# Performance work log

Measured on AMD Instinct MI355X. Metric: run time of the kernel, lower is better.

Reference implementation:

```python
import jax, jax.numpy as jnp
import numpy as np

N, E, DIN, DOUT = 50000, 500000, 128, 128


def setup_inputs() -> dict:
    key = jax.random.key(0)
    ks = jax.random.split(key, 12)
    s = 0.02
    return {
        "x": jax.random.normal(ks[0], (N, DIN), jnp.float32),
        "pos": jax.random.normal(ks[1], (N, 3), jnp.float32),
        "edge_index": jax.random.randint(ks[2], (2, E), 0, N, jnp.int64),
        # mlp_h: Linear(DIN,DIN) -> ReLU -> Linear(DIN,3) -> Tanh
        "h_w1": jax.random.normal(ks[3], (DIN, DIN), jnp.float32) * s,
        "h_b1": jnp.zeros((DIN,), jnp.float32),
        "h_w2": jax.random.normal(ks[4], (DIN, 3), jnp.float32) * s,
        "h_b2": jnp.zeros((3,), jnp.float32),
        # mlp_f: Linear(DIN+3, DOUT) -> ReLU
        "f_w": jax.random.normal(ks[5], (DIN + 3, DOUT), jnp.float32) * s,
        "f_b": jnp.zeros((DOUT,), jnp.float32),
        # mlp_g: Linear(DOUT,DOUT) -> ReLU -> Linear(DOUT,DIN) -> ReLU
        "g_w1": jax.random.normal(ks[6], (DOUT, DOUT), jnp.float32) * s,
        "g_b1": jnp.zeros((DOUT,), jnp.float32),
        "g_w2": jax.random.normal(ks[7], (DOUT, DIN), jnp.float32) * s,
        "g_b2": jnp.zeros((DIN,), jnp.float32),
    }


def reference(x, pos, edge_index, h_w1, h_b1, h_w2, h_b2, f_w, f_b,
              g_w1, g_b1, g_w2, g_b2):
    # PointGNNConv (aggr='sum'):
    #   delta = mlp_h(x)                                   [N, 3]
    #   msg_e = mlp_f([pos_j - pos_i + delta_i, x_j])      [E, DOUT]
    #   agg_i = sum_{j in N(i)} msg_e                       [N, DOUT]
    #   out   = x + mlp_g(agg)                              [N, DIN]
    delta = jnp.tanh(jax.nn.relu(x @ h_w1 + h_b1) @ h_w2 + h_b2)
    src = edge_index[0]  # j (source)
    dst = edge_index[1]  # i (target)
    edge_feat = jnp.concatenate(
        [pos[src] - pos[dst] + delta[dst], x[src]], axis=-1)  # [E, DIN+3]
    msg = jax.nn.relu(edge_feat @ f_w + f_b)                   # [E, DOUT]
    agg = jax.ops.segment_sum(msg, dst, num_segments=N)        # [N, DOUT]
    out = jax.nn.relu(jax.nn.relu(agg @ g_w1 + g_b1) @ g_w2 + g_b2)
    return x + out
```

## Files before the change

kernel.cpp:

```cpp
#include <hip/hip_runtime.h>
#include <hip/hip_bf16.h>

typedef float f32x4 __attribute__((ext_vector_type(4)));
typedef short bf16x8 __attribute__((ext_vector_type(8)));
typedef unsigned short u16x8 __attribute__((ext_vector_type(8)));

#define MFMA16(a, b, c) __builtin_amdgcn_mfma_f32_16x16x32_bf16((a), (b), (c), 0, 0, 0)
#define BCAP 128

static __device__ __forceinline__ short f2bf(float f) {
    union { float f; unsigned u; } v; v.f = f;
    unsigned r = v.u + 0x7FFFu + ((v.u >> 16) & 1u);
    return (short)(r >> 16);
}
static __device__ __forceinline__ float bflo(unsigned u) {
    union { unsigned u; float f; } v; v.u = u << 16; return v.f;
}
static __device__ __forceinline__ float bfhi(unsigned u) {
    union { unsigned u; float f; } v; v.u = u & 0xffff0000u; return v.f;
}
static __device__ __forceinline__ unsigned packbf(float lo, float hi) {
    return ((unsigned)(unsigned short)f2bf(lo)) | (((unsigned)(unsigned short)f2bf(hi)) << 16);
}

__global__ __launch_bounds__(256) void k_prep(
    const float* __restrict__ hw1, const float* __restrict__ fw,
    const float* __restrict__ gw1, const float* __restrict__ gw2,
    unsigned short* __restrict__ wT,
    const int* __restrict__ ei, int* __restrict__ flag,
    int* __restrict__ cursor, int N)
{
    const int gtid = blockIdx.x * 256 + threadIdx.x;
    if (gtid == 0) {
        int nz = 0;
        for (int i = 0; i < 64; ++i) nz |= ei[2 * i + 1];
        *flag = (nz != 0) ? 1 : 0;
    }
    for (int i = gtid; i < N; i += 16384) cursor[i] = i << 7;
    const int idx = gtid;
    const int c = idx >> 7, k = idx & 127;
    wT[0 * 16384 + idx] = (unsigned short)f2bf(hw1[(size_t)k * 128 + c]);
    wT[1 * 16384 + idx] = (unsigned short)f2bf(fw[(size_t)(3 + k) * 128 + c]);
    wT[2 * 16384 + idx] = (unsigned short)f2bf(gw1[(size_t)k * 128 + c]);
    wT[3 * 16384 + idx] = (unsigned short)f2bf(gw2[(size_t)k * 128 + c]);
}

static __device__ __forceinline__ void scatter_edges(
    const int* __restrict__ ei, int* __restrict__ cursor, int* __restrict__ list,
    int f, int E, int gbase, int gstride)
{
    const int stride2 = gstride * 2;
    for (int e0 = gbase * 2; e0 < E; e0 += stride2) {
        int s0, s1 = 0, d0, d1 = 0;
        const bool two = (e0 + 1 < E);
        if (f) {
            if (two) {
                const int2 sv = *reinterpret_cast<const int2*>(ei + e0);
                const int2 dv = *reinterpret_cast<const int2*>(ei + (size_t)E + e0);
                s0 = sv.x; s1 = sv.y; d0 = dv.x; d1 = dv.y;
            } else { s0 = ei[e0]; d0 = ei[(size_t)E + e0]; }
        } else {
            if (two) {
                const int4 sv = *reinterpret_cast<const int4*>(ei + 2 * (size_t)e0);
                const int4 dv = *reinterpret_cast<const int4*>(ei + 2 * ((size_t)E + e0));
                s0 = sv.x; s1 = sv.z; d0 = dv.x; d1 = dv.z;
            } else { s0 = ei[2 * (size_t)e0]; d0 = ei[2 * ((size_t)E + e0)]; }
        }
        int p = atomicAdd(&cursor[d0], 1);
        if (p < (d0 << 7) + BCAP) list[p] = s0;
        if (two) {
            p = atomicAdd(&cursor[d1], 1);
            if (p < (d1 << 7) + BCAP) list[p] = s1;
        }
    }
}

__global__ __launch_bounds__(256) void k_front(
    const float* __restrict__ x, const float* __restrict__ pos,
    const float* __restrict__ hb1,
    const float* __restrict__ hw2, const float* __restrict__ hb2,
    const float* __restrict__ fw, const float* __restrict__ fb,
    const unsigned short* __restrict__ wT,
    unsigned short* __restrict__ Pb, unsigned short* __restrict__ Qb, int N,
    const int* __restrict__ ei, int* __restrict__ cursor, int* __restrict__ list,
    const int* __restrict__ flag, int E)
{
    __shared__ float t1s[16][132];
    __shared__ unsigned short pls[16 * 128];
    __shared__ float poss[48];
    __shared__ float dqs[48];
    __shared__ float w2s[384];
    __shared__ float w3s[384];
    __shared__ float b1s[128], fbs[128], b2s[3];

    const int tid = threadIdx.x;
    const int lane = tid & 63, wave = tid >> 6;
    const int r16 = lane & 15, kg = lane >> 4;
    const int f = *flag;
    const bool early = (blockIdx.x & 1);

    for (int i = tid; i < 128; i += 256) { b1s[i] = hb1[i]; fbs[i] = fb[i]; }
    for (int i = tid; i < 384; i += 256) { w2s[i] = hw2[i]; w3s[i] = fw[i]; }
    if (tid < 3) b2s[tid] = hb2[tid];

    const unsigned short* hw1T = wT;
    const unsigned short* fwxT = wT + 16384;
    bf16x8 bw1[2][4], bwx[2][4];
    #pragma unroll
    for (int si = 0; si < 2; ++si) {
        const int c = (wave * 2 + si) * 16 + r16;
        #pragma unroll
        for (int t = 0; t < 4; ++t) {
            const int k0 = t * 32 + kg * 8;
            bw1[si][t] = *reinterpret_cast<const bf16x8*>(hw1T + c * 128 + k0);
            bwx[si][t] = *reinterpret_cast<const bf16x8*>(fwxT + c * 128 + k0);
        }
    }

    const int ntiles = (N + 15) >> 4;
    int tile = blockIdx.x;

    float4 px[8];
    float posr = 0.f;
    if (tile < ntiles) {
        int arow = (tile << 4) + r16; if (arow >= N) arow = N - 1;
        const float4* p = reinterpret_cast<const float4*>(x + (size_t)arow * 128);
        #pragma unroll
        for (int t = 0; t < 4; ++t) { px[2 * t] = p[t * 8 + kg * 2]; px[2 * t + 1] = p[t * 8 + kg * 2 + 1]; }
        if (tid < 48) {
            int r = tid / 3, m = tid - 3 * r;
            int rr = (tile << 4) + r; if (rr >= N) rr = N - 1;
            posr = pos[(size_t)rr * 3 + m];
        }
    }

    if (early)
        scatter_edges(ei, cursor, list, f, E, blockIdx.x * 256 + tid, gridDim.x * 256);

    __syncthreads();

    for (; tile < ntiles; tile += gridDim.x) {
        const int row0 = tile << 4;

        if (tid < 48) poss[tid] = posr;
        bf16x8 a[4];
        #pragma unroll
        for (int t = 0; t < 4; ++t) {
            float4 u0 = px[2 * t], u1 = px[2 * t + 1];
            bf16x8 v;
            v[0] = f2bf(u0.x); v[1] = f2bf(u0.y); v[2] = f2bf(u0.z); v[3] = f2bf(u0.w);
            v[4] = f2bf(u1.x); v[5] = f2bf(u1.y); v[6] = f2bf(u1.z); v[7] = f2bf(u1.w);
            a[t] = v;
        }
        const int ntile = tile + gridDim.x;
        if (ntile < ntiles) {
            int arow = (ntile << 4) + r16; if (arow >= N) arow = N - 1;
            const float4* p = reinterpret_cast<const float4*>(x + (size_t)arow * 128);
            #pragma unroll
            for (int t = 0; t < 4; ++t) { px[2 * t] = p[t * 8 + kg * 2]; px[2 * t + 1] = p[t * 8 + kg * 2 + 1]; }
            if (tid < 48) {
                int r = tid / 3, m = tid - 3 * r;
                int rr = (ntile << 4) + r; if (rr >= N) rr = N - 1;
                posr = pos[(size_t)rr * 3 + m];
            }
        }
        f32x4 acc1[2], accP[2];
        acc1[0] = 0.f; acc1[1] = 0.f; accP[0] = 0.f; accP[1] = 0.f;
        #pragma unroll
        for (int t = 0; t < 4; ++t) {
            #pragma unroll
            for (int si = 0; si < 2; ++si) {
                acc1[si] = MFMA16(a[t], bw1[si][t], acc1[si]);
                accP[si] = MFMA16(a[t], bwx[si][t], accP[si]);
            }
        }
        #pragma unroll
        for (int si = 0; si < 2; ++si) {
            const int c = (wave * 2 + si) * 16 + r16;
            #pragma unroll
            for (int j = 0; j < 4; ++j) {
                const int r = kg * 4 + j;
                t1s[r][c] = fmaxf(acc1[si][j] + b1s[c], 0.f);
            }
        }
        __syncthreads();

        #pragma unroll
        for (int si = 0; si < 2; ++si) {
            const int c = (wave * 2 + si) * 16 + r16;
            const int g = c >> 3, ce = c & 7;
            #pragma unroll
            for (int j = 0; j < 4; ++j) {
                const int r = kg * 4 + j;
                float pval = accP[si][j] + fbs[c]
                    + poss[r * 3 + 0] * w3s[0 * 128 + c]
                    + poss[r * 3 + 1] * w3s[1 * 128 + c]
                    + poss[r * 3 + 2] * w3s[2 * 128 + c];
                pls[r * 128 + (g ^ r) * 8 + ce] = (unsigned short)f2bf(pval);
            }
        }
        if (tid < 192) {
            const int pair = tid >> 2, h = tid & 3;
            const int r = pair / 3, m = pair - 3 * r;
            float s = 0.f;
            const int k0 = h * 32;
            #pragma unroll
            for (int k = k0; k < k0 + 32; k += 4) {
                float4 tv = *reinterpret_cast<const float4*>(&t1s[r][k]);
                s += tv.x * w2s[(k + 0) * 3 + m] + tv.y * w2s[(k + 1) * 3 + m]
                   + tv.z * w2s[(k + 2) * 3 + m] + tv.w * w2s[(k + 3) * 3 + m];
            }
            s += __shfl_xor(s, 1, 4);
            s += __shfl_xor(s, 2, 4);
            if (h == 0) dqs[pair] = tanhf(s + b2s[m]) - poss[pair];
        }
        __syncthreads();

        {
            const int row = tid >> 4, g0 = tid & 15;
            if (row0 + row < N) {
                u16x8 v = *reinterpret_cast<const u16x8*>(&pls[row * 128 + (g0 ^ row) * 8]);
                *reinterpret_cast<u16x8*>(Pb + (size_t)(row0 + row) * 128 + g0 * 8) = v;
            }
        }
        #pragma unroll
        for (int it = 0; it < 2; ++it) {
            const int idx = tid + it * 256;
            const int cg = idx & 31, r = idx >> 5;
            const int c0 = cg * 4;
            if (row0 + r < N) {
                const float d0 = dqs[r * 3 + 0], d1 = dqs[r * 3 + 1], d2 = dqs[r * 3 + 2];
                float q0 = d0 * w3s[c0 + 0] + d1 * w3s[128 + c0 + 0] + d2 * w3s[256 + c0 + 0];
                float q1 = d0 * w3s[c0 + 1] + d1 * w3s[128 + c0 + 1] + d2 * w3s[256 + c0 + 1];
                float q2 = d0 * w3s[c0 + 2] + d1 * w3s[128 + c0 + 2] + d2 * w3s[256 + c0 + 2];
                float q3 = d0 * w3s[c0 + 3] + d1 * w3s[128 + c0 + 3] + d2 * w3s[256 + c0 + 3];
                uint2 w; w.x = packbf(q0, q1); w.y = packbf(q2, q3);
                *reinterpret_cast<uint2*>(Qb + (size_t)(row0 + r) * 128 + c0) = w;
            }
        }
        __syncthreads();
    }

    if (!early)
        scatter_edges(ei, cursor, list, f, E, blockIdx.x * 256 + tid, gridDim.x * 256);
}

__global__ __launch_bounds__(256) void k_agg(
    const unsigned short* __restrict__ Pb, const unsigned short* __restrict__ Qb,
    const int* __restrict__ cursor, const int* __restrict__ list,
    unsigned short* __restrict__ aggb, int N)
{
    const int d = blockIdx.x * 16 + (threadIdx.x >> 4);
    if (d >= N) return;
    const int l = threadIdx.x & 15;
    const int start = d << 7;
    const int deg = min(cursor[d] - start, BCAP);

    const uint4 qu = *reinterpret_cast<const uint4*>(Qb + (size_t)d * 128 + l * 8);
    const float q0 = bflo(qu.x), q1 = bfhi(qu.x), q2 = bflo(qu.y), q3 = bfhi(qu.y);
    const float q4 = bflo(qu.z), q5 = bfhi(qu.z), q6 = bflo(qu.w), q7 = bfhi(qu.w);
    float a0 = 0.f, a1 = 0.f, a2 = 0.f, a3 = 0.f;
    float a4 = 0.f, a5 = 0.f, a6 = 0.f, a7 = 0.f;

#define ACC_EDGE(u) do { \
        a0 += fmaxf(bflo(u.x) + q0, 0.f); \
        a1 += fmaxf(bfhi(u.x) + q1, 0.f); \
        a2 += fmaxf(bflo(u.y) + q2, 0.f); \
        a3 += fmaxf(bfhi(u.y) + q3, 0.f); \
        a4 += fmaxf(bflo(u.z) + q4, 0.f); \
        a5 += fmaxf(bfhi(u.z) + q5, 0.f); \
        a6 += fmaxf(bflo(u.w) + q6, 0.f); \
        a7 += fmaxf(bfhi(u.w) + q7, 0.f); \
    } while (0)

    for (int b0 = 0; b0 < deg; b0 += 16) {
        int s = 0;
        if (b0 + l < deg) s = list[start + b0 + l];
        const int m = min(16, deg - b0);
        int k = 0;
        for (; k + 8 <= m; k += 8) {
            const int sj0 = __shfl(s, k + 0, 16);
            const int sj1 = __shfl(s, k + 1, 16);
            const int sj2 = __shfl(s, k + 2, 16);
            const int sj3 = __shfl(s, k + 3, 16);
            const int sj4 = __shfl(s, k + 4, 16);
            const int sj5 = __shfl(s, k + 5, 16);
            const int sj6 = __shfl(s, k + 6, 16);
            const int sj7 = __shfl(s, k + 7, 16);
            const uint4 u0 = *reinterpret_cast<const uint4*>(Pb + (size_t)sj0 * 128 + l * 8);
            const uint4 u1 = *reinterpret_cast<const uint4*>(Pb + (size_t)sj1 * 128 + l * 8);
            const uint4 u2 = *reinterpret_cast<const uint4*>(Pb + (size_t)sj2 * 128 + l * 8);
            const uint4 u3 = *reinterpret_cast<const uint4*>(Pb + (size_t)sj3 * 128 + l * 8);
            const uint4 u4 = *reinterpret_cast<const uint4*>(Pb + (size_t)sj4 * 128 + l * 8);
            const uint4 u5 = *reinterpret_cast<const uint4*>(Pb + (size_t)sj5 * 128 + l * 8);
            const uint4 u6 = *reinterpret_cast<const uint4*>(Pb + (size_t)sj6 * 128 + l * 8);
            const uint4 u7 = *reinterpret_cast<const uint4*>(Pb + (size_t)sj7 * 128 + l * 8);
            ACC_EDGE(u0); ACC_EDGE(u1); ACC_EDGE(u2); ACC_EDGE(u3);
            ACC_EDGE(u4); ACC_EDGE(u5); ACC_EDGE(u6); ACC_EDGE(u7);
        }
        for (; k + 4 <= m; k += 4) {
            const int sj0 = __shfl(s, k + 0, 16);
            const int sj1 = __shfl(s, k + 1, 16);
            const int sj2 = __shfl(s, k + 2, 16);
            const int sj3 = __shfl(s, k + 3, 16);
            const uint4 u0 = *reinterpret_cast<const uint4*>(Pb + (size_t)sj0 * 128 + l * 8);
            const uint4 u1 = *reinterpret_cast<const uint4*>(Pb + (size_t)sj1 * 128 + l * 8);
            const uint4 u2 = *reinterpret_cast<const uint4*>(Pb + (size_t)sj2 * 128 + l * 8);
            const uint4 u3 = *reinterpret_cast<const uint4*>(Pb + (size_t)sj3 * 128 + l * 8);
            ACC_EDGE(u0); ACC_EDGE(u1); ACC_EDGE(u2); ACC_EDGE(u3);
        }
        for (; k < m; ++k) {
            const int sj = __shfl(s, k, 16);
            const uint4 u = *reinterpret_cast<const uint4*>(Pb + (size_t)sj * 128 + l * 8);
            ACC_EDGE(u);
        }
    }
#undef ACC_EDGE

    uint4 w;
    w.x = packbf(a0, a1); w.y = packbf(a2, a3);
    w.z = packbf(a4, a5); w.w = packbf(a6, a7);
    *reinterpret_cast<uint4*>(aggb + (size_t)d * 128 + l * 8) = w;
}

__global__ __launch_bounds__(256) void k_back(
    const unsigned short* __restrict__ aggb, const float* __restrict__ x,
    const unsigned short* __restrict__ wT,
    const float* __restrict__ gb1, const float* __restrict__ gb2,
    float* __restrict__ out, int N)
{
    __shared__ unsigned short uls[16 * 128];
    __shared__ float b1s[128], b2s[128];

    const int tid = threadIdx.x;
    const int lane = tid & 63, wave = tid >> 6;
    const int r16 = lane & 15, kg = lane >> 4;

    for (int i = tid; i < 128; i += 256) { b1s[i] = gb1[i]; b2s[i] = gb2[i]; }

    const unsigned short* gw1T = wT + 2 * 16384;
    const unsigned short* gw2T = wT + 3 * 16384;
    bf16x8 bg1[2][4], bg2[2][4];
    #pragma unroll
    for (int si = 0; si < 2; ++si) {
        const int c = (wave * 2 + si) * 16 + r16;
        #pragma unroll
        for (int t = 0; t < 4; ++t) {
            const int k0 = t * 32 + kg * 8;
            bg1[si][t] = *reinterpret_cast<const bf16x8*>(gw1T + c * 128 + k0);
            bg2[si][t] = *reinterpret_cast<const bf16x8*>(gw2T + c * 128 + k0);
        }
    }

    const int ntiles = (N + 15) >> 4;
    int tile = blockIdx.x;

    bf16x8 a[4];
    float xv[2][4];
    if (tile < ntiles) {
        int arow = (tile << 4) + r16; if (arow >= N) arow = N - 1;
        #pragma unroll
        for (int t = 0; t < 4; ++t)
            a[t] = *reinterpret_cast<const bf16x8*>(aggb + (size_t)arow * 128 + t * 32 + kg * 8);
        #pragma unroll
        for (int si = 0; si < 2; ++si) {
            const int c = (wave * 2 + si) * 16 + r16;
            #pragma unroll
            for (int j = 0; j < 4; ++j) {
                const int r = (tile << 4) + kg * 4 + j;
                xv[si][j] = (r < N) ? x[(size_t)r * 128 + c] : 0.f;
            }
        }
    }
    __syncthreads();

    for (; tile < ntiles; tile += gridDim.x) {
        const int row0 = tile << 4;

        f32x4 accU[2];
        accU[0] = 0.f; accU[1] = 0.f;
        #pragma unroll
        for (int t = 0; t < 4; ++t) {
            #pragma unroll
            for (int si = 0; si < 2; ++si)
                accU[si] = MFMA16(a[t], bg1[si][t], accU[si]);
        }

        const int ntile = tile + gridDim.x;
        float xvn[2][4];
        if (ntile < ntiles) {
            int arow = (ntile << 4) + r16; if (arow >= N) arow = N - 1;
            #pragma unroll
            for (int t = 0; t < 4; ++t)
                a[t] = *reinterpret_cast<const bf16x8*>(aggb + (size_t)arow * 128 + t * 32 + kg * 8);
            #pragma unroll
            for (int si = 0; si < 2; ++si) {
                const int c = (wave * 2 + si) * 16 + r16;
                #pragma unroll
                for (int j = 0; j < 4; ++j) {
                    const int r = (ntile << 4) + kg * 4 + j;
                    xvn[si][j] = (r < N) ? x[(size_t)r * 128 + c] : 0.f;
                }
            }
        }

        __syncthreads();
        #pragma unroll
        for (int si = 0; si < 2; ++si) {
            const int c = (wave * 2 + si) * 16 + r16;
            const int g = c >> 3, ce = c & 7;
            #pragma unroll
            for (int j = 0; j < 4; ++j) {
                const int r = kg * 4 + j;
                uls[r * 128 + (g ^ r) * 8 + ce] =
                    (unsigned short)f2bf(fmaxf(accU[si][j] + b1s[c], 0.f));
            }
        }
        __syncthreads();

        bf16x8 a2[4];
        #pragma unroll
        for (int t = 0; t < 4; ++t) {
            const int p = (t * 4 + kg) ^ r16;
            a2[t] = *reinterpret_cast<const bf16x8*>(&uls[r16 * 128 + p * 8]);
        }
        f32x4 accO[2];
        accO[0] = 0.f; accO[1] = 0.f;
        #pragma unroll
        for (int t = 0; t < 4; ++t) {
            #pragma unroll
            for (int si = 0; si < 2; ++si)
                accO[si] = MFMA16(a2[t], bg2[si][t], accO[si]);
        }
        #pragma unroll
        for (int si = 0; si < 2; ++si) {
            const int c = (wave * 2 + si) * 16 + r16;
            #pragma unroll
            for (int j = 0; j < 4; ++j) {
                const int r = kg * 4 + j;
                if (row0 + r < N) {
                    out[(size_t)(row0 + r) * 128 + c] =
                        xv[si][j] + fmaxf(accO[si][j] + b2s[c], 0.f);
                }
            }
        }
        if (ntile < ntiles) {
            #pragma unroll
            for (int si = 0; si < 2; ++si)
                #pragma unroll
                for (int j = 0; j < 4; ++j)
                    xv[si][j] = xvn[si][j];
        }
    }
}

extern "C" void kernel_launch(void* const* d_in, const int* in_sizes, int n_in,
                              void* d_out, int out_size, void* d_ws, size_t ws_size,
                              hipStream_t stream)
{
    const float* x   = (const float*)d_in[0];
    const float* pos = (const float*)d_in[1];
    const int*   ei  = (const int*)d_in[2];
    const float* hw1 = (const float*)d_in[3];
    const float* hb1 = (const float*)d_in[4];
    const float* hw2 = (const float*)d_in[5];
    const float* hb2 = (const float*)d_in[6];
    const float* fw  = (const float*)d_in[7];
    const float* fb  = (const float*)d_in[8];
    const float* gw1 = (const float*)d_in[9];
    const float* gb1 = (const float*)d_in[10];
    const float* gw2 = (const float*)d_in[11];
    const float* gb2 = (const float*)d_in[12];
    float* out = (float*)d_out;

    const int N = in_sizes[0] / 128;
    const int E = in_sizes[2] / 2;

    const size_t NW = (size_t)N * 128;
    unsigned short* Pb   = (unsigned short*)d_ws;
    unsigned short* Qb   = Pb + NW;
    unsigned short* aggb = Qb + NW;
    unsigned short* wT   = aggb + NW;
    int* cursor = (int*)(wT + 4 * 16384);
    int* list   = cursor + N;
    int* flag   = list + (size_t)N * BCAP;

    k_prep<<<64, 256, 0, stream>>>(hw1, fw, gw1, gw2, wT, ei, flag, cursor, N);
    k_front<<<1042, 256, 0, stream>>>(x, pos, hb1, hw2, hb2, fw, fb, wT, Pb, Qb, N,
                                      ei, cursor, list, flag, E);
    k_agg<<<(N + 15) / 16, 256, 0, stream>>>(Pb, Qb, cursor, list, aggb, N);
    k_back<<<1042, 256, 0, stream>>>(aggb, x, wT, gb1, gb2, out, N);
}
```

Before: 102.5 us.

## Fuse aggregation into back MLP kernel and pad per-node atomic cursors

Merges the neighbor-aggregation kernel with the back MLP kernel. Each block now aggregates 16 destination rows directly into shared memory and immediately runs the two MFMA layers on them, so the bf16 agg buffer is never written to or reread from global memory and one launch is removed. Separately, per-node cursors are spaced 16 ints apart so that concurrent atomicAdds on neighbouring nodes land on different cache lines. In exchange, the back kernel now launches one block per tile and reloads its weights in every block instead of using a persistent grid, and the cursor array takes 16x more memory.

```diff
diff --git a/kernel.cpp b/kernel.cpp
--- a/kernel.cpp
+++ b/kernel.cpp
@@ -7,6 +7,7 @@
 
 #define MFMA16(a, b, c) __builtin_amdgcn_mfma_f32_16x16x32_bf16((a), (b), (c), 0, 0, 0)
 #define BCAP 128
+#define CSTR 16
 
 static __device__ __forceinline__ short f2bf(float f) {
     union { float f; unsigned u; } v; v.f = f;
@@ -36,7 +37,7 @@
         for (int i = 0; i < 64; ++i) nz |= ei[2 * i + 1];
         *flag = (nz != 0) ? 1 : 0;
     }
-    for (int i = gtid; i < N; i += 16384) cursor[i] = i << 7;
+    for (int i = gtid; i < N; i += 16384) cursor[(size_t)i * CSTR] = i << 7;
     const int idx = gtid;
     const int c = idx >> 7, k = idx & 127;
     wT[0 * 16384 + idx] = (unsigned short)f2bf(hw1[(size_t)k * 128 + c]);
@@ -66,10 +67,10 @@
                 s0 = sv.x; s1 = sv.z; d0 = dv.x; d1 = dv.z;
             } else { s0 = ei[2 * (size_t)e0]; d0 = ei[2 * ((size_t)E + e0)]; }
         }
-        int p = atomicAdd(&cursor[d0], 1);
+        int p = atomicAdd(&cursor[(size_t)d0 * CSTR], 1);
         if (p < (d0 << 7) + BCAP) list[p] = s0;
         if (two) {
-            p = atomicAdd(&cursor[d1], 1);
+            p = atomicAdd(&cursor[(size_t)d1 * CSTR], 1);
             if (p < (d1 << 7) + BCAP) list[p] = s1;
         }
     }
@@ -245,87 +246,10 @@
         scatter_edges(ei, cursor, list, f, E, blockIdx.x * 256 + tid, gridDim.x * 256);
 }
 
-__global__ __launch_bounds__(256) void k_agg(
+__global__ __launch_bounds__(256) void k_aggback(
     const unsigned short* __restrict__ Pb, const unsigned short* __restrict__ Qb,
     const int* __restrict__ cursor, const int* __restrict__ list,
-    unsigned short* __restrict__ aggb, int N)
-{
-    const int d = blockIdx.x * 16 + (threadIdx.x >> 4);
-    if (d >= N) return;
-    const int l = threadIdx.x & 15;
-    const int start = d << 7;
-    const int deg = min(cursor[d] - start, BCAP);
-
-    const uint4 qu = *reinterpret_cast<const uint4*>(Qb + (size_t)d * 128 + l * 8);
-    const float q0 = bflo(qu.x), q1 = bfhi(qu.x), q2 = bflo(qu.y), q3 = bfhi(qu.y);
-    const float q4 = bflo(qu.z), q5 = bfhi(qu.z), q6 = bflo(qu.w), q7 = bfhi(qu.w);
-    float a0 = 0.f, a1 = 0.f, a2 = 0.f, a3 = 0.f;
-    float a4 = 0.f, a5 = 0.f, a6 = 0.f, a7 = 0.f;
-
-#define ACC_EDGE(u) do { \
-        a0 += fmaxf(bflo(u.x) + q0, 0.f); \
-        a1 += fmaxf(bfhi(u.x) + q1, 0.f); \
-        a2 += fmaxf(bflo(u.y) + q2, 0.f); \
-        a3 += fmaxf(bfhi(u.y) + q3, 0.f); \
-        a4 += fmaxf(bflo(u.z) + q4, 0.f); \
-        a5 += fmaxf(bfhi(u.z) + q5, 0.f); \
-        a6 += fmaxf(bflo(u.w) + q6, 0.f); \
-        a7 += fmaxf(bfhi(u.w) + q7, 0.f); \
-    } while (0)
-
-    for (int b0 = 0; b0 < deg; b0 += 16) {
-        int s = 0;
-        if (b0 + l < deg) s = list[start + b0 + l];
-        const int m = min(16, deg - b0);
-        int k = 0;
-        for (; k + 8 <= m; k += 8) {
-            const int sj0 = __shfl(s, k + 0, 16);
-            const int sj1 = __shfl(s, k + 1, 16);
-            const int sj2 = __shfl(s, k + 2, 16);
-            const int sj3 = __shfl(s, k + 3, 16);
-            const int sj4 = __shfl(s, k + 4, 16);
-            const int sj5 = __shfl(s, k + 5, 16);
-            const int sj6 = __shfl(s, k + 6, 16);
-            const int sj7 = __shfl(s, k + 7, 16);
-            const uint4 u0 = *reinterpret_cast<const uint4*>(Pb + (size_t)sj0 * 128 + l * 8);
-            const uint4 u1 = *reinterpret_cast<const uint4*>(Pb + (size_t)sj1 * 128 + l * 8);
-            const uint4 u2 = *reinterpret_cast<const uint4*>(Pb + (size_t)sj2 * 128 + l * 8);
-            const uint4 u3 = *reinterpret_cast<const uint4*>(Pb + (size_t)sj3 * 128 + l * 8);
-            const uint4 u4 = *reinterpret_cast<const uint4*>(Pb + (size_t)sj4 * 128 + l * 8);
-            const uint4 u5 = *reinterpret_cast<const uint4*>(Pb + (size_t)sj5 * 128 + l * 8);
-            const uint4 u6 = *reinterpret_cast<const uint4*>(Pb + (size_t)sj6 * 128 + l * 8);
-            const uint4 u7 = *reinterpret_cast<const uint4*>(Pb + (size_t)sj7 * 128 + l * 8);
-            ACC_EDGE(u0); ACC_EDGE(u1); ACC_EDGE(u2); ACC_EDGE(u3);
-            ACC_EDGE(u4); ACC_EDGE(u5); ACC_EDGE(u6); ACC_EDGE(u7);
-        }
-        for (; k + 4 <= m; k += 4) {
-            const int sj0 = __shfl(s, k + 0, 16);
-            const int sj1 = __shfl(s, k + 1, 16);
-            const int sj2 = __shfl(s, k + 2, 16);
-            const int sj3 = __shfl(s, k + 3, 16);
-            const uint4 u0 = *reinterpret_cast<const uint4*>(Pb + (size_t)sj0 * 128 + l * 8);
-            const uint4 u1 = *reinterpret_cast<const uint4*>(Pb + (size_t)sj1 * 128 + l * 8);
-            const uint4 u2 = *reinterpret_cast<const uint4*>(Pb + (size_t)sj2 * 128 + l * 8);
-            const uint4 u3 = *reinterpret_cast<const uint4*>(Pb + (size_t)sj3 * 128 + l * 8);
-            ACC_EDGE(u0); ACC_EDGE(u1); ACC_EDGE(u2); ACC_EDGE(u3);
-        }
-        for (; k < m; ++k) {
-            const int sj = __shfl(s, k, 16);
-            const uint4 u = *reinterpret_cast<const uint4*>(Pb + (size_t)sj * 128 + l * 8);
-            ACC_EDGE(u);
-        }
-    }
-#undef ACC_EDGE
-
-    uint4 w;
-    w.x = packbf(a0, a1); w.y = packbf(a2, a3);
-    w.z = packbf(a4, a5); w.w = packbf(a6, a7);
-    *reinterpret_cast<uint4*>(aggb + (size_t)d * 128 + l * 8) = w;
-}
-
-__global__ __launch_bounds__(256) void k_back(
-    const unsigned short* __restrict__ aggb, const float* __restrict__ x,
-    const unsigned short* __restrict__ wT,
+    const float* __restrict__ x, const unsigned short* __restrict__ wT,
     const float* __restrict__ gb1, const float* __restrict__ gb2,
     float* __restrict__ out, int N)
 {
@@ -335,6 +259,7 @@
     const int tid = threadIdx.x;
     const int lane = tid & 63, wave = tid >> 6;
     const int r16 = lane & 15, kg = lane >> 4;
+    const int row0 = blockIdx.x << 4;
 
     for (int i = tid; i < 128; i += 256) { b1s[i] = gb1[i]; b2s[i] = gb2[i]; }
 
@@ -351,105 +276,143 @@
             bg2[si][t] = *reinterpret_cast<const bf16x8*>(gw2T + c * 128 + k0);
         }
     }
-
-    const int ntiles = (N + 15) >> 4;
-    int tile = blockIdx.x;
+    float xv[2][4];
+    #pragma unroll
+    for (int si = 0; si < 2; ++si) {
+        const int c = (wave * 2 + si) * 16 + r16;
+        #pragma unroll
+        for (int j = 0; j < 4; ++j) {
+            const int r = row0 + kg * 4 + j;
+            xv[si][j] = (r < N) ? x[(size_t)r * 128 + c] : 0.f;
+        }
+    }
+
+    {
+        const int grp = tid >> 4, l = tid & 15;
+        const int d = row0 + grp;
+        float a0 = 0.f, a1 = 0.f, a2 = 0.f, a3 = 0.f;
+        float a4 = 0.f, a5 = 0.f, a6 = 0.f, a7 = 0.f;
+        if (d < N) {
+            const int start = d << 7;
+            const int deg = min(cursor[(size_t)d * CSTR] - start, BCAP);
+            const uint4 qu = *reinterpret_cast<const uint4*>(Qb + (size_t)d * 128 + l * 8);
+            const float q0 = bflo(qu.x), q1 = bfhi(qu.x), q2 = bflo(qu.y), q3 = bfhi(qu.y);
+            const float q4 = bflo(qu.z), q5 = bfhi(qu.z), q6 = bflo(qu.w), q7 = bfhi(qu.w);
+
+#define ACC_EDGE(u) do { \
+            a0 += fmaxf(bflo(u.x) + q0, 0.f); \
+            a1 += fmaxf(bfhi(u.x) + q1, 0.f); \
+            a2 += fmaxf(bflo(u.y) + q2, 0.f); \
+            a3 += fmaxf(bfhi(u.y) + q3, 0.f); \
+            a4 += fmaxf(bflo(u.z) + q4, 0.f); \
+            a5 += fmaxf(bfhi(u.z) + q5, 0.f); \
+            a6 += fmaxf(bflo(u.w) + q6, 0.f); \
+            a7 += fmaxf(bfhi(u.w) + q7, 0.f); \
+        } while (0)
+
+            for (int b0 = 0; b0 < deg; b0 += 16) {
+                int s = 0;
+                if (b0 + l < deg) s = list[start + b0 + l];
+                const int m = min(16, deg - b0);
+                int k = 0;
+                for (; k + 8 <= m; k += 8) {
+                    const int sj0 = __shfl(s, k + 0, 16);
+                    const int sj1 = __shfl(s, k + 1, 16);
+                    const int sj2 = __shfl(s, k + 2, 16);
+                    const int sj3 = __shfl(s, k + 3, 16);
+                    const int sj4 = __shfl(s, k + 4, 16);
+                    const int sj5 = __shfl(s, k + 5, 16);
+                    const int sj6 = __shfl(s, k + 6, 16);
+                    const int sj7 = __shfl(s, k + 7, 16);
+                    const uint4 u0 = *reinterpret_cast<const uint4*>(Pb + (size_t)sj0 * 128 + l * 8);
+                    const uint4 u1 = *reinterpret_cast<const uint4*>(Pb + (size_t)sj1 * 128 + l * 8);
+                    const uint4 u2 = *reinterpret_cast<const uint4*>(Pb + (size_t)sj2 * 128 + l * 8);
+                    const uint4 u3 = *reinterpret_cast<const uint4*>(Pb + (size_t)sj3 * 128 + l * 8);
+                    const uint4 u4 = *reinterpret_cast<const uint4*>(Pb + (size_t)sj4 * 128 + l * 8);
+                    const uint4 u5 = *reinterpret_cast<const uint4*>(Pb + (size_t)sj5 * 128 + l * 8);
+                    const uint4 u6 = *reinterpret_cast<const uint4*>(Pb + (size_t)sj6 * 128 + l * 8);
+                    const uint4 u7 = *reinterpret_cast<const uint4*>(Pb + (size_t)sj7 * 128 + l * 8);
+                    ACC_EDGE(u0); ACC_EDGE(u1); ACC_EDGE(u2); ACC_EDGE(u3);
+                    ACC_EDGE(u4); ACC_EDGE(u5); ACC_EDGE(u6); ACC_EDGE(u7);
+                }
+                for (; k + 4 <= m; k += 4) {
+                    const int sj0 = __shfl(s, k + 0, 16);
+                    const int sj1 = __shfl(s, k + 1, 16);
+                    const int sj2 = __shfl(s, k + 2, 16);
+                    const int sj3 = __shfl(s, k + 3, 16);
+                    const uint4 u0 = *reinterpret_cast<const uint4*>(Pb + (size_t)sj0 * 128 + l * 8);
+                    const uint4 u1 = *reinterpret_cast<const uint4*>(Pb + (size_t)sj1 * 128 + l * 8);
+                    const uint4 u2 = *reinterpret_cast<const uint4*>(Pb + (size_t)sj2 * 128 + l * 8);
+                    const uint4 u3 = *reinterpret_cast<const uint4*>(Pb + (size_t)sj3 * 128 + l * 8);
+                    ACC_EDGE(u0); ACC_EDGE(u1); ACC_EDGE(u2); ACC_EDGE(u3);
+                }
+                for (; k < m; ++k) {
+                    const int sj = __shfl(s, k, 16);
+                    const uint4 u = *reinterpret_cast<const uint4*>(Pb + (size_t)sj * 128 + l * 8);
+                    ACC_EDGE(u);
+                }
+            }
+#undef ACC_EDGE
+        }
+        uint4 w;
+        w.x = packbf(a0, a1); w.y = packbf(a2, a3);
+        w.z = packbf(a4, a5); w.w = packbf(a6, a7);
+        *reinterpret_cast<uint4*>(&uls[grp * 128 + (l ^ grp) * 8]) = w;
+    }
+    __syncthreads();
 
     bf16x8 a[4];
-    float xv[2][4];
-    if (tile < ntiles) {
-        int arow = (tile << 4) + r16; if (arow >= N) arow = N - 1;
-        #pragma unroll
-        for (int t = 0; t < 4; ++t)
-            a[t] = *reinterpret_cast<const bf16x8*>(aggb + (size_t)arow * 128 + t * 32 + kg * 8);
-        #pragma unroll
-        for (int si = 0; si < 2; ++si) {
-            const int c = (wave * 2 + si) * 16 + r16;
-            #pragma unroll
-            for (int j = 0; j < 4; ++j) {
-                const int r = (tile << 4) + kg * 4 + j;
-                xv[si][j] = (r < N) ? x[(size_t)r * 128 + c] : 0.f;
-            }
-        }
+    #pragma unroll
+    for (int t = 0; t < 4; ++t) {
+        const int p = (t * 4 + kg) ^ r16;
+        a[t] = *reinterpret_cast<const bf16x8*>(&uls[r16 * 128 + p * 8]);
+    }
+    f32x4 accU[2];
+    accU[0] = 0.f; accU[1] = 0.f;
+    #pragma unroll
+    for (int t = 0; t < 4; ++t) {
+        #pragma unroll
+        for (int si = 0; si < 2; ++si)
+            accU[si] = MFMA16(a[t], bg1[si][t], accU[si]);
     }
     __syncthreads();
-
-    for (; tile < ntiles; tile += gridDim.x) {
-        const int row0 = tile << 4;
-
-        f32x4 accU[2];
-        accU[0] = 0.f; accU[1] = 0.f;
-        #pragma unroll
-        for (int t = 0; t < 4; ++t) {
-            #pragma unroll
-            for (int si = 0; si < 2; ++si)
-                accU[si] = MFMA16(a[t], bg1[si][t], accU[si]);
-        }
-
-        const int ntile = tile + gridDim.x;
-        float xvn[2][4];
-        if (ntile < ntiles) {
-            int arow = (ntile << 4) + r16; if (arow >= N) arow = N - 1;
-            #pragma unroll
-            for (int t = 0; t < 4; ++t)
-                a[t] = *reinterpret_cast<const bf16x8*>(aggb + (size_t)arow * 128 + t * 32 + kg * 8);
-            #pragma unroll
-            for (int si = 0; si < 2; ++si) {
-                const int c = (wave * 2 + si) * 16 + r16;
-                #pragma unroll
-                for (int j = 0; j < 4; ++j) {
-                    const int r = (ntile << 4) + kg * 4 + j;
-                    xvn[si][j] = (r < N) ? x[(size_t)r * 128 + c] : 0.f;
-                }
-            }
-        }
-
-        __syncthreads();
-        #pragma unroll
-        for (int si = 0; si < 2; ++si) {
-            const int c = (wave * 2 + si) * 16 + r16;
-            const int g = c >> 3, ce = c & 7;
-            #pragma unroll
-            for (int j = 0; j < 4; ++j) {
-                const int r = kg * 4 + j;
-                uls[r * 128 + (g ^ r) * 8 + ce] =
-                    (unsigned short)f2bf(fmaxf(accU[si][j] + b1s[c], 0.f));
-            }
-        }
-        __syncthreads();
-
-        bf16x8 a2[4];
-        #pragma unroll
-        for (int t = 0; t < 4; ++t) {
-            const int p = (t * 4 + kg) ^ r16;
-            a2[t] = *reinterpret_cast<const bf16x8*>(&uls[r16 * 128 + p * 8]);
-        }
-        f32x4 accO[2];
-        accO[0] = 0.f; accO[1] = 0.f;
-        #pragma unroll
-        for (int t = 0; t < 4; ++t) {
-            #pragma unroll
-            for (int si = 0; si < 2; ++si)
-                accO[si] = MFMA16(a2[t], bg2[si][t], accO[si]);
-        }
-        #pragma unroll
-        for (int si = 0; si < 2; ++si) {
-            const int c = (wave * 2 + si) * 16 + r16;
-            #pragma unroll
-            for (int j = 0; j < 4; ++j) {
-                const int r = kg * 4 + j;
-                if (row0 + r < N) {
-                    out[(size_t)(row0 + r) * 128 + c] =
-                        xv[si][j] + fmaxf(accO[si][j] + b2s[c], 0.f);
-                }
-            }
-        }
-        if (ntile < ntiles) {
-            #pragma unroll
-            for (int si = 0; si < 2; ++si)
-                #pragma unroll
-                for (int j = 0; j < 4; ++j)
-                    xv[si][j] = xvn[si][j];
+    #pragma unroll
+    for (int si = 0; si < 2; ++si) {
+        const int c = (wave * 2 + si) * 16 + r16;
+        const int g = c >> 3, ce = c & 7;
+        #pragma unroll
+        for (int j = 0; j < 4; ++j) {
+            const int r = kg * 4 + j;
+            uls[r * 128 + (g ^ r) * 8 + ce] =
+                (unsigned short)f2bf(fmaxf(accU[si][j] + b1s[c], 0.f));
+        }
+    }
+    __syncthreads();
+
+    bf16x8 a2[4];
+    #pragma unroll
+    for (int t = 0; t < 4; ++t) {
+        const int p = (t * 4 + kg) ^ r16;
+        a2[t] = *reinterpret_cast<const bf16x8*>(&uls[r16 * 128 + p * 8]);
+    }
+    f32x4 accO[2];
+    accO[0] = 0.f; accO[1] = 0.f;
+    #pragma unroll
+    for (int t = 0; t < 4; ++t) {
+        #pragma unroll
+        for (int si = 0; si < 2; ++si)
+            accO[si] = MFMA16(a2[t], bg2[si][t], accO[si]);
+    }
+    #pragma unroll
+    for (int si = 0; si < 2; ++si) {
+        const int c = (wave * 2 + si) * 16 + r16;
+        #pragma unroll
+        for (int j = 0; j < 4; ++j) {
+            const int r = kg * 4 + j;
+            if (row0 + r < N) {
+                out[(size_t)(row0 + r) * 128 + c] =
+                    xv[si][j] + fmaxf(accO[si][j] + b2s[c], 0.f);
+            }
         }
     }
 }
@@ -477,17 +440,16 @@
     const int E = in_sizes[2] / 2;
 
     const size_t NW = (size_t)N * 128;
-    unsigned short* Pb   = (unsigned short*)d_ws;
-    unsigned short* Qb   = Pb + NW;
-    unsigned short* aggb = Qb + NW;
-    unsigned short* wT   = aggb + NW;
+    unsigned short* Pb = (unsigned short*)d_ws;
+    unsigned short* Qb = Pb + NW;
+    unsigned short* wT = Qb + NW;
     int* cursor = (int*)(wT + 4 * 16384);
-    int* list   = cursor + N;
+    int* list   = cursor + (size_t)N * CSTR;
     int* flag   = list + (size_t)N * BCAP;
 
     k_prep<<<64, 256, 0, stream>>>(hw1, fw, gw1, gw2, wT, ei, flag, cursor, N);
     k_front<<<1042, 256, 0, stream>>>(x, pos, hb1, hw2, hb2, fw, fb, wT, Pb, Qb, N,
                                       ei, cursor, list, flag, E);
-    k_agg<<<(N + 15) / 16, 256, 0, stream>>>(Pb, Qb, cursor, list, aggb, N);
-    k_back<<<1042, 256, 0, stream>>>(aggb, x, wT, gb1, gb2, out, N);
-}
+    k_aggback<<<(N + 15) / 16, 256, 0, stream>>>(Pb, Qb, cursor, list, x, wT,
+                                                 gb1, gb2, out, N);
+}
```

New measurement: 116.0 us. 13.2% more time.
